# Performance work log

Measured on AMD Instinct MI355X. Metric: run time of the kernel, lower is better.

## Reference

```python
import jax, jax.numpy as jnp
import numpy as np

N_NODES = 50000
N_EDGES = 800000
IN_DIM = 256
OUT_DIM = 64
HEADS = 4
NEG_SLOPE = 0.2  # PyG GATConv default


def setup_inputs() -> dict:
    key = jax.random.key(0)
    k1, k2, k3, k4, k5, k6 = jax.random.split(key, 6)
    x = jax.random.normal(k1, (N_NODES, IN_DIM), dtype=jnp.float32)
    edge_index = jax.random.randint(k2, (2, N_EDGES), 0, N_NODES, dtype=jnp.int64)
    scale = 1.0 / np.sqrt(IN_DIM)
    W = jax.random.normal(k3, (IN_DIM, HEADS * OUT_DIM), dtype=jnp.float32) * scale
    att_src = jax.random.normal(k4, (HEADS, OUT_DIM), dtype=jnp.float32) * scale
    att_dst = jax.random.normal(k5, (HEADS, OUT_DIM), dtype=jnp.float32) * scale
    bias = jnp.zeros((HEADS * OUT_DIM,), dtype=jnp.float32)
    return {"x": x, "edge_index": edge_index, "W": W,
            "att_src": att_src, "att_dst": att_dst, "bias": bias}


def reference(x, edge_index, W, att_src, att_dst, bias):
    N = x.shape[0]
    H, C = att_src.shape
    # add self loops (PyG GATConv default add_self_loops=True)
    loop = jnp.arange(N, dtype=edge_index.dtype)
    src = jnp.concatenate([edge_index[0], loop])  # [E+N] source j
    dst = jnp.concatenate([edge_index[1], loop])  # [E+N] target i
    # linear projection, per-head features  [N, H, C]
    h = (x @ W).reshape(N, H, C)
    # attention logits: a_src . h_j + a_dst . h_i  -> [E, H]
    a_src = jnp.einsum('nhc,hc->nh', h, att_src)
    a_dst = jnp.einsum('nhc,hc->nh', h, att_dst)
    e = jax.nn.leaky_relu(a_src[src] + a_dst[dst], negative_slope=NEG_SLOPE)
    # edge softmax over incoming edges of each destination node
    m = jax.ops.segment_max(e, dst, num_segments=N)          # [N, H]
    p = jnp.exp(e - m[dst])                                  # [E, H]
    denom = jax.ops.segment_sum(p, dst, num_segments=N)      # [N, H]
    alpha = p / (denom[dst] + 1e-16)                         # [E, H]
    # weighted scatter-aggregate of gathered source features
    out = jax.ops.segment_sum(alpha[:, :, None] * h[src], dst, num_segments=N)
    out = out.reshape(N, H * C) + bias
    return jax.nn.relu(out)  # GATLayer active_func
```

## Files before the change

kernel.cpp:

```cpp
#include <hip/hip_runtime.h>

constexpr int N  = 50000;
constexpr int E  = 800000;
constexpr int K  = 256;
constexpr int F  = 256;
constexpr int H  = 4;
constexpr float SLOPE = 0.2f;

constexpr int CAPS = 6;

constexpr int NBK  = 98;
constexpr int BCAP = 16384;
constexpr int BKB  = 256;
constexpr int EPB  = E / BKB;

constexpr int WT_ROWS = 272;

constexpr size_t OFF_HB   = 0;
constexpr size_t OFF_WT   = OFF_HB   + (size_t)N * F * 2;
constexpr size_t OFF_ASRC = OFF_WT   + (size_t)WT_ROWS * K * 2;
constexpr size_t OFF_ADST = OFF_ASRC + (size_t)N * H * 4;
constexpr size_t OFF_DEG  = OFF_ADST + (size_t)N * H * 4;
constexpr size_t OFF_FLAG = OFF_DEG  + (size_t)N * 4;
constexpr size_t OFF_CSR  = OFF_FLAG + 64;
constexpr size_t OFF_BUF  = OFF_CSR  + (size_t)N * 64 * 4;
constexpr size_t OFF_GCUR = OFF_BUF  + (size_t)NBK * BCAP * 4;

constexpr int GEMM_TILES  = (N + 127) / 128;
constexpr int GEMM_BLOCKS = GEMM_TILES * 2;

typedef short short8 __attribute__((ext_vector_type(8)));
typedef float floatx4 __attribute__((ext_vector_type(4)));

__device__ __forceinline__ float leaky(float x) {
    return fmaxf(x, SLOPE * x);
}
__device__ __forceinline__ float blo(unsigned u) { return __uint_as_float(u << 16); }
__device__ __forceinline__ float bhi(unsigned u) { return __uint_as_float(u & 0xffff0000u); }
__device__ __forceinline__ unsigned short f2b(float f) {
    unsigned u = __float_as_uint(f);
    return (unsigned short)((u + 0x7fffu + ((u >> 16) & 1u)) >> 16);
}
__device__ __forceinline__ unsigned pk2(float a, float b) {
    return (unsigned)f2b(a) | ((unsigned)f2b(b) << 16);
}

__device__ __forceinline__ int edge_at(const void* ei, int is64, size_t i) {
    if (is64) return (int)((const long long*)ei)[i];
    return ((const int*)ei)[i];
}

__global__ __launch_bounds__(256)
void prep(const float* __restrict__ Wm, const float* __restrict__ att_src,
          const float* __restrict__ att_dst, const unsigned* __restrict__ ei_words,
          unsigned short* __restrict__ Wt, int* __restrict__ flag,
          int* __restrict__ gcur) {
    __shared__ float tile[64][65];
    __shared__ float as_l[64], ad_l[64];
    const int bid = blockIdx.x;
    const int t = threadIdx.x;
    if (bid < 16) {
        const int k0 = (bid & 3) * 64;
        const int n0 = (bid >> 2) * 64;
        const int r = t >> 2;
        const int c4 = (t & 3) * 16;
        #pragma unroll
        for (int i = 0; i < 16; i += 4) {
            float4 v = *reinterpret_cast<const float4*>(
                Wm + (size_t)(k0 + r) * F + n0 + c4 + i);
            tile[r][c4 + i + 0] = v.x;
            tile[r][c4 + i + 1] = v.y;
            tile[r][c4 + i + 2] = v.z;
            tile[r][c4 + i + 3] = v.w;
        }
        __syncthreads();
        unsigned pk[8];
        #pragma unroll
        for (int j = 0; j < 8; ++j)
            pk[j] = pk2(tile[c4 + 2 * j + 0][r], tile[c4 + 2 * j + 1][r]);
        unsigned short* dst = Wt + (size_t)(n0 + r) * K + k0 + c4;
        *reinterpret_cast<uint4*>(dst)     = make_uint4(pk[0], pk[1], pk[2], pk[3]);
        *reinterpret_cast<uint4*>(dst + 8) = make_uint4(pk[4], pk[5], pk[6], pk[7]);
    } else if (bid < 20) {
        const int h = bid - 16;
        if (t < 64) {
            as_l[t] = att_src[h * 64 + t];
            ad_l[t] = att_dst[h * 64 + t];
        }
        __syncthreads();
        const int k = t;
        const float* wr = Wm + (size_t)k * F + h * 64;
        float s = 0.f, d = 0.f;
        #pragma unroll
        for (int c = 0; c < 64; c += 4) {
            float4 w = *reinterpret_cast<const float4*>(wr + c);
            s += w.x * as_l[c] + w.y * as_l[c + 1]
               + w.z * as_l[c + 2] + w.w * as_l[c + 3];
            d += w.x * ad_l[c] + w.y * ad_l[c + 1]
               + w.z * ad_l[c + 2] + w.w * ad_l[c + 3];
        }
        Wt[(size_t)(256 + h) * K + k] = f2b(s);
        Wt[(size_t)(260 + h) * K + k] = f2b(d);
        if (h == 0) {
            #pragma unroll
            for (int r = 0; r < 8; ++r) Wt[(size_t)(264 + r) * K + k] = 0;
        }
    } else {
        if (t < 64) {
            unsigned v = ei_words[2 * t + 1];
            unsigned long long b = __ballot(v != 0u);
            if (t == 0) *flag = (b == 0ull) ? 1 : 0;
        }
        for (int j = t; j < NBK * 16; j += 256) gcur[j] = 0;
    }
}

constexpr int LDA = 72;
constexpr int LDW = 72;

__global__ __launch_bounds__(512, 4)
void gemm_hist(const float* __restrict__ X, const unsigned short* __restrict__ Wt,
               unsigned short* __restrict__ Hb, float* __restrict__ asrc,
               float* __restrict__ adst, const void* __restrict__ ei,
               const int* __restrict__ flag, unsigned* __restrict__ buf,
               int* __restrict__ gcur) {
    __shared__ unsigned short Al[128 * LDA];
    __shared__ unsigned short Wl[144 * LDW];
    const int tid = threadIdx.x;

    if (blockIdx.x < BKB) {
        int* cnt = (int*)(void*)Al;
        int* gsh = cnt + 128;
        int* scn = gsh + 128;
        unsigned* staged = (unsigned*)(void*)Wl;
        const int is64 = *flag;
        const int e0 = blockIdx.x * EPB;
        if (tid < 128) cnt[tid] = 0;
        __syncthreads();
        for (int it = 0; it < (EPB + 511) / 512; ++it) {
            int idx = it * 512 + tid;
            if (idx < EPB) {
                int d = edge_at(ei, is64, (size_t)E + e0 + idx);
                atomicAdd(&cnt[d >> 9], 1);
            }
        }
        __syncthreads();
        if (tid < 128) scn[tid] = cnt[tid];
        __syncthreads();
        for (int off = 1; off < 128; off <<= 1) {
            int v = 0;
            if (tid < 128 && tid >= off) v = scn[tid - off];
            __syncthreads();
            if (tid < 128) scn[tid] += v;
            __syncthreads();
        }
        if (tid < 128) {
            int c = cnt[tid];
            int lbase = scn[tid] - c;
            int gb = 0;
            if (c > 0 && tid < NBK) gb = atomicAdd(&gcur[tid * 16], c);
            gsh[tid] = gb - lbase;
            cnt[tid] = lbase;
        }
        __syncthreads();
        for (int it = 0; it < (EPB + 511) / 512; ++it) {
            int idx = it * 512 + tid;
            if (idx < EPB) {
                int d = edge_at(ei, is64, (size_t)E + e0 + idx);
                int s = edge_at(ei, is64, (size_t)(e0 + idx));
                int bk = d >> 9;
                int slot = atomicAdd(&cnt[bk], 1);
                staged[slot] = ((unsigned)bk << 25)
                             | ((unsigned)(d & 511) << 16) | (unsigned)s;
            }
        }
        __syncthreads();
        for (int j = tid; j < EPB; j += 512) {
            unsigned v = staged[j];
            int bk = (int)(v >> 25);
            buf[(size_t)bk * BCAP + gsh[bk] + j] = v;
        }
        return;
    }

    const int bid = blockIdx.x - BKB;
    const int tileR = bid >> 1;
    const int halfC = bid & 1;
    const int m0 = tileR * 128;
    const int c0 = halfC * 128;

    const int wv = tid >> 6, lane = tid & 63;
    const int quad = lane >> 4, l15 = lane & 15;
    const int rH = wv >> 2;
    const int cQ = wv & 3;
    const bool fusedw = (halfC == 1) && (cQ == 3);

    floatx4 acc[4][2];
    #pragma unroll
    for (int i = 0; i < 4; ++i)
        #pragma unroll
        for (int j = 0; j < 2; ++j) acc[i][j] = (floatx4)0.f;
    floatx4 accf[4];
    #pragma unroll
    for (int i = 0; i < 4; ++i) accf[i] = (floatx4)0.f;

    const int ar = tid >> 2;
    const int akc = (tid & 3) * 16;
    const bool arow_ok = (m0 + ar) < N;
    const int wr = tid >> 2;
    const int wkc = (tid & 3) * 16;

    for (int k0 = 0; k0 < K; k0 += 64) {
        {
            const float* src = X + (size_t)(m0 + ar) * K + k0 + akc;
            unsigned short* dst = &Al[ar * LDA + akc];
            #pragma unroll
            for (int i = 0; i < 16; i += 4) {
                float4 v = arow_ok ? *reinterpret_cast<const float4*>(src + i)
                                   : make_float4(0.f, 0.f, 0.f, 0.f);
                *reinterpret_cast<uint2*>(dst + i) =
                    make_uint2(pk2(v.x, v.y), pk2(v.z, v.w));
            }
        }
        {
            const unsigned short* src = Wt + (size_t)(c0 + wr) * K + k0 + wkc;
            unsigned short* dst = &Wl[wr * LDW + wkc];
            *reinterpret_cast<int4*>(dst)     = *reinterpret_cast<const int4*>(src);
            *reinterpret_cast<int4*>(dst + 8) = *reinterpret_cast<const int4*>(src + 8);
        }
        if (halfC == 1 && tid < 64) {
            const int fr = tid >> 2;
            const int fk = (tid & 3) * 16;
            const unsigned short* src = Wt + (size_t)(256 + fr) * K + k0 + fk;
            unsigned short* dst = &Wl[(128 + fr) * LDW + fk];
            *reinterpret_cast<int4*>(dst)     = *reinterpret_cast<const int4*>(src);
            *reinterpret_cast<int4*>(dst + 8) = *reinterpret_cast<const int4*>(src + 8);
        }
        __syncthreads();
        #pragma unroll
        for (int kk = 0; kk < 64; kk += 32) {
            short8 a[4];
            #pragma unroll
            for (int i = 0; i < 4; ++i)
                a[i] = *reinterpret_cast<const short8*>(
                    &Al[(rH * 64 + i * 16 + l15) * LDA + kk + quad * 8]);
            #pragma unroll
            for (int j = 0; j < 2; ++j) {
                short8 b = *reinterpret_cast<const short8*>(
                    &Wl[(cQ * 32 + j * 16 + l15) * LDW + kk + quad * 8]);
                #pragma unroll
                for (int i = 0; i < 4; ++i)
                    acc[i][j] = __builtin_amdgcn_mfma_f32_16x16x32_bf16(
                        a[i], b, acc[i][j], 0, 0, 0);
            }
            if (fusedw) {
                short8 bf = *reinterpret_cast<const short8*>(
                    &Wl[(128 + l15) * LDW + kk + quad * 8]);
                #pragma unroll
                for (int i = 0; i < 4; ++i)
                    accf[i] = __builtin_amdgcn_mfma_f32_16x16x32_bf16(
                        a[i], bf, accf[i], 0, 0, 0);
            }
        }
        __syncthreads();
    }
    #pragma unroll
    for (int i = 0; i < 4; ++i) {
        const int row = m0 + rH * 64 + i * 16 + quad * 4;
        #pragma unroll
        for (int j = 0; j < 2; ++j) {
            const int colb = c0 + cQ * 32 + j * 16;
            #pragma unroll
            for (int r = 0; r < 4; ++r) {
                float v = acc[i][j][r];
                float vn = __shfl_xor(v, 1);
                unsigned p = pk2(v, vn);
                unsigned q = __shfl_xor(p, 2);
                if ((l15 & 3) == 0 && (row + r) < N) {
                    *reinterpret_cast<uint2*>(
                        &Hb[(size_t)(row + r) * F + colb + l15]) =
                        make_uint2(p, q);
                }
            }
        }
    }
    if (fusedw) {
        #pragma unroll
        for (int i = 0; i < 4; ++i) {
            const int rbase = m0 + rH * 64 + i * 16 + quad * 4;
            #pragma unroll
            for (int r = 0; r < 4; ++r) {
                int row = rbase + r;
                if (row < N) {
                    if (l15 < 4)      asrc[row * H + l15] = accf[i][r];
                    else if (l15 < 8) adst[row * H + (l15 - 4)] = accf[i][r];
                }
            }
        }
    }
}

__global__ __launch_bounds__(1024)
void rank_scatter(const unsigned* __restrict__ buf, const int* __restrict__ gcur,
                  int* __restrict__ csr, int* __restrict__ deg) {
    __shared__ int h[512];
    const int b = blockIdx.x;
    const int t = threadIdx.x;
    if (t < 512) h[t] = 0;
    __syncthreads();
    const int nb = gcur[b * 16];
    for (int j = t; j < nb; j += 1024) {
        unsigned v = buf[(size_t)b * BCAP + j];
        int dl = (int)((v >> 16) & 511u);
        int s  = (int)(v & 0xffffu);
        int r = atomicAdd(&h[dl], 1);
        csr[(((b << 9) + dl) << CAPS) + r] = s;
    }
    __syncthreads();
    if (t < 512) {
        int n0 = (b << 9) + t;
        if (n0 < N) deg[n0] = h[t];
    }
}

__global__ __launch_bounds__(256, 8)
void aggregate(const unsigned short* __restrict__ Hb, const float* __restrict__ asrc,
               const float* __restrict__ adst, const int* __restrict__ deg,
               const int* __restrict__ csr, const float* __restrict__ bias,
               float* __restrict__ out) {
    const int wv = threadIdx.x >> 6;
    const int lane = threadIdx.x & 63;
    const int half = lane >> 5;
    const int l32 = lane & 31;
    const int hd = l32 >> 3;
    const int node = blockIdx.x * 4 + wv;

    const char* hbase = (const char*)Hb;
    const char* abase = (const char*)asrc;
    const unsigned lsh = (unsigned)l32 << 4;
    const unsigned hsh = (unsigned)hd << 2;

    const float adsti = adst[node * H + hd];
    const int start = node << CAPS;
    const int end = start + deg[node];

    float denom = 0.f;
    float a0 = 0.f, a1 = 0.f, a2 = 0.f, a3 = 0.f;
    float a4 = 0.f, a5 = 0.f, a6 = 0.f, a7 = 0.f;
    int e = start;
    for (; e + 8 <= end; e += 8) {
        unsigned s[4]; float l[4]; uint4 u[4];
        #pragma unroll
        for (int j = 0; j < 4; ++j) s[j] = (unsigned)csr[e + 2 * j + half];
        #pragma unroll
        for (int j = 0; j < 4; ++j)
            l[j] = *(const float*)(abase + ((s[j] << 4) + hsh));
        #pragma unroll
        for (int j = 0; j < 4; ++j)
            u[j] = *(const uint4*)(hbase + ((s[j] << 9) + lsh));
        #pragma unroll
        for (int j = 0; j < 4; ++j) {
            float p = __expf(leaky(l[j] + adsti));
            denom += p;
            a0 += p * blo(u[j].x); a1 += p * bhi(u[j].x);
            a2 += p * blo(u[j].y); a3 += p * bhi(u[j].y);
            a4 += p * blo(u[j].z); a5 += p * bhi(u[j].z);
            a6 += p * blo(u[j].w); a7 += p * bhi(u[j].w);
        }
    }
    for (; e + 2 <= end; e += 2) {
        unsigned s0 = (unsigned)csr[e + half];
        float l0 = *(const float*)(abase + ((s0 << 4) + hsh));
        uint4 u0 = *(const uint4*)(hbase + ((s0 << 9) + lsh));
        float p = __expf(leaky(l0 + adsti));
        denom += p;
        a0 += p * blo(u0.x); a1 += p * bhi(u0.x);
        a2 += p * blo(u0.y); a3 += p * bhi(u0.y);
        a4 += p * blo(u0.z); a5 += p * bhi(u0.z);
        a6 += p * blo(u0.w); a7 += p * bhi(u0.w);
    }
    {
        const int rem = end - e;
        bool active;
        unsigned sf;
        if (half == 0) { active = (rem == 1); sf = active ? (unsigned)csr[e] : 0u; }
        else           { active = true;       sf = (unsigned)node; }
        if (active) {
            float l0 = *(const float*)(abase + ((sf << 4) + hsh));
            uint4 u0 = *(const uint4*)(hbase + ((sf << 9) + lsh));
            float p = __expf(leaky(l0 + adsti));
            denom += p;
            a0 += p * blo(u0.x); a1 += p * bhi(u0.x);
            a2 += p * blo(u0.y); a3 += p * bhi(u0.y);
            a4 += p * blo(u0.z); a5 += p * bhi(u0.z);
            a6 += p * blo(u0.w); a7 += p * bhi(u0.w);
        }
    }
    a0 += __shfl_xor(a0, 32); a1 += __shfl_xor(a1, 32);
    a2 += __shfl_xor(a2, 32); a3 += __shfl_xor(a3, 32);
    a4 += __shfl_xor(a4, 32); a5 += __shfl_xor(a5, 32);
    a6 += __shfl_xor(a6, 32); a7 += __shfl_xor(a7, 32);
    denom += __shfl_xor(denom, 32);
    if (half == 0) {
        const float inv = 1.f / (denom + 1e-16f);
        float4 b0 = *reinterpret_cast<const float4*>(bias + l32 * 8);
        float4 b1 = *reinterpret_cast<const float4*>(bias + l32 * 8 + 4);
        float4 o0, o1;
        o0.x = fmaxf(a0 * inv + b0.x, 0.f);
        o0.y = fmaxf(a1 * inv + b0.y, 0.f);
        o0.z = fmaxf(a2 * inv + b0.z, 0.f);
        o0.w = fmaxf(a3 * inv + b0.w, 0.f);
        o1.x = fmaxf(a4 * inv + b1.x, 0.f);
        o1.y = fmaxf(a5 * inv + b1.y, 0.f);
        o1.z = fmaxf(a6 * inv + b1.z, 0.f);
        o1.w = fmaxf(a7 * inv + b1.w, 0.f);
        float* orow = out + (size_t)node * F + l32 * 8;
        *reinterpret_cast<float4*>(orow)     = o0;
        *reinterpret_cast<float4*>(orow + 4) = o1;
    }
}

extern "C" void kernel_launch(void* const* d_in, const int* in_sizes, int n_in,
                              void* d_out, int out_size, void* d_ws, size_t ws_size,
                              hipStream_t stream) {
    const float* x       = (const float*)d_in[0];
    const void*  ei      = d_in[1];
    const float* Wm      = (const float*)d_in[2];
    const float* att_src = (const float*)d_in[3];
    const float* att_dst = (const float*)d_in[4];
    const float* bias    = (const float*)d_in[5];
    float* out = (float*)d_out;

    char* ws = (char*)d_ws;
    unsigned short* hb = (unsigned short*)(ws + OFF_HB);
    unsigned short* wt = (unsigned short*)(ws + OFF_WT);
    float* asrc = (float*)(ws + OFF_ASRC);
    float* adst = (float*)(ws + OFF_ADST);
    int* deg  = (int*)(ws + OFF_DEG);
    int* flag = (int*)(ws + OFF_FLAG);
    int* csr  = (int*)(ws + OFF_CSR);
    unsigned* buf = (unsigned*)(ws + OFF_BUF);
    int* gcur = (int*)(ws + OFF_GCUR);

    prep<<<21, 256, 0, stream>>>(Wm, att_src, att_dst, (const unsigned*)ei,
                                 wt, flag, gcur);
    gemm_hist<<<BKB + GEMM_BLOCKS, 512, 0, stream>>>(
        x, wt, hb, asrc, adst, ei, flag, buf, gcur);
    rank_scatter<<<NBK, 1024, 0, stream>>>(buf, gcur, csr, deg);
    aggregate<<<N / 4, 256, 0, stream>>>(hb, asrc, adst, deg, csr, bias, out);
}
```

Measured before the change: 214.9 us.

## Restage pipeline: move edge bucketing into prep, fuse rank-scatter with GEMM

Edge bucketing moves from the GEMM kernel into the prep kernel, which also converts X to bf16 in a separate pass. The rank/scatter CSR build now runs as extra blocks of the GEMM kernel, so one launch is removed and CSR construction overlaps with the matmul. The GEMM then loads pre-converted bf16 X instead of converting fp32 on the fly, and gcur is zeroed with a memset. The trade-off is an extra full read and write of X (bf16 copy) and an extra memset call, plus a staged buffer that now sits in the smaller 256-thread block's shared tile.

```diff
diff --git a/kernel.cpp b/kernel.cpp
--- a/kernel.cpp
+++ b/kernel.cpp
@@ -21,13 +21,16 @@
 constexpr size_t OFF_ASRC = OFF_WT   + (size_t)WT_ROWS * K * 2;
 constexpr size_t OFF_ADST = OFF_ASRC + (size_t)N * H * 4;
 constexpr size_t OFF_DEG  = OFF_ADST + (size_t)N * H * 4;
-constexpr size_t OFF_FLAG = OFF_DEG  + (size_t)N * 4;
-constexpr size_t OFF_CSR  = OFF_FLAG + 64;
+constexpr size_t OFF_CSR  = OFF_DEG  + (size_t)N * 4 + 64;
 constexpr size_t OFF_BUF  = OFF_CSR  + (size_t)N * 64 * 4;
 constexpr size_t OFF_GCUR = OFF_BUF  + (size_t)NBK * BCAP * 4;
+constexpr size_t OFF_XB   = OFF_GCUR + (size_t)NBK * 16 * 4;
 
 constexpr int GEMM_TILES  = (N + 127) / 128;
 constexpr int GEMM_BLOCKS = GEMM_TILES * 2;
+
+constexpr int CVT_BLOCKS  = 1600;
+constexpr int PREP_BLOCKS = BKB + 20 + CVT_BLOCKS;
 
 typedef short short8 __attribute__((ext_vector_type(8)));
 typedef float floatx4 __attribute__((ext_vector_type(4)));
@@ -51,17 +54,73 @@
 }
 
 __global__ __launch_bounds__(256)
-void prep(const float* __restrict__ Wm, const float* __restrict__ att_src,
-          const float* __restrict__ att_dst, const unsigned* __restrict__ ei_words,
-          unsigned short* __restrict__ Wt, int* __restrict__ flag,
-          int* __restrict__ gcur) {
+void prep_all(const float* __restrict__ Wm, const float* __restrict__ att_src,
+              const float* __restrict__ att_dst, const void* __restrict__ ei,
+              const float* __restrict__ X, unsigned short* __restrict__ Wt,
+              unsigned short* __restrict__ Xb, unsigned* __restrict__ buf,
+              int* __restrict__ gcur) {
     __shared__ float tile[64][65];
     __shared__ float as_l[64], ad_l[64];
     const int bid = blockIdx.x;
     const int t = threadIdx.x;
-    if (bid < 16) {
-        const int k0 = (bid & 3) * 64;
-        const int n0 = (bid >> 2) * 64;
+    if (bid < BKB) {
+        const unsigned* ew = (const unsigned*)ei;
+        unsigned hw = ew[2 * (t & 63) + 1];
+        const int is64 = (__ballot(hw != 0u) == 0ull) ? 1 : 0;
+        int* cnt = (int*)(void*)tile;
+        int* gsh = cnt + 128;
+        int* scn = gsh + 128;
+        unsigned* staged = (unsigned*)(scn + 128);
+        const int e0 = bid * EPB;
+        if (t < 128) cnt[t] = 0;
+        __syncthreads();
+        for (int it = 0; it < (EPB + 255) / 256; ++it) {
+            int idx = it * 256 + t;
+            if (idx < EPB) {
+                int d = edge_at(ei, is64, (size_t)E + e0 + idx);
+                atomicAdd(&cnt[d >> 9], 1);
+            }
+        }
+        __syncthreads();
+        if (t < 128) scn[t] = cnt[t];
+        __syncthreads();
+        for (int off = 1; off < 128; off <<= 1) {
+            int v = 0;
+            if (t < 128 && t >= off) v = scn[t - off];
+            __syncthreads();
+            if (t < 128) scn[t] += v;
+            __syncthreads();
+        }
+        if (t < 128) {
+            int c = cnt[t];
+            int lbase = scn[t] - c;
+            int gb = 0;
+            if (c > 0 && t < NBK) gb = atomicAdd(&gcur[t * 16], c);
+            gsh[t] = gb - lbase;
+            cnt[t] = lbase;
+        }
+        __syncthreads();
+        for (int it = 0; it < (EPB + 255) / 256; ++it) {
+            int idx = it * 256 + t;
+            if (idx < EPB) {
+                int d = edge_at(ei, is64, (size_t)E + e0 + idx);
+                int s = edge_at(ei, is64, (size_t)(e0 + idx));
+                int bk = d >> 9;
+                int slot = atomicAdd(&cnt[bk], 1);
+                staged[slot] = ((unsigned)bk << 25)
+                             | ((unsigned)(d & 511) << 16) | (unsigned)s;
+            }
+        }
+        __syncthreads();
+        for (int j = t; j < EPB; j += 256) {
+            unsigned v = staged[j];
+            int bk = (int)(v >> 25);
+            buf[(size_t)bk * BCAP + gsh[bk] + j] = v;
+        }
+    } else if (bid < BKB + 16) {
+        const int tb = bid - BKB;
+        const int k0 = (tb & 3) * 64;
+        const int n0 = (tb >> 2) * 64;
         const int r = t >> 2;
         const int c4 = (t & 3) * 16;
         #pragma unroll
@@ -81,8 +140,8 @@
         unsigned short* dst = Wt + (size_t)(n0 + r) * K + k0 + c4;
         *reinterpret_cast<uint4*>(dst)     = make_uint4(pk[0], pk[1], pk[2], pk[3]);
         *reinterpret_cast<uint4*>(dst + 8) = make_uint4(pk[4], pk[5], pk[6], pk[7]);
-    } else if (bid < 20) {
-        const int h = bid - 16;
+    } else if (bid < BKB + 20) {
+        const int h = bid - (BKB + 16);
         if (t < 64) {
             as_l[t] = att_src[h * 64 + t];
             ad_l[t] = att_dst[h * 64 + t];
@@ -106,12 +165,15 @@
             for (int r = 0; r < 8; ++r) Wt[(size_t)(264 + r) * K + k] = 0;
         }
     } else {
-        if (t < 64) {
-            unsigned v = ei_words[2 * t + 1];
-            unsigned long long b = __ballot(v != 0u);
-            if (t == 0) *flag = (b == 0ull) ? 1 : 0;
-        }
-        for (int j = t; j < NBK * 16; j += 256) gcur[j] = 0;
+        const int cb = bid - (BKB + 20);
+        const float4* X4 = reinterpret_cast<const float4*>(X);
+        uint4* XB4 = reinterpret_cast<uint4*>(Xb);
+        const int NK8 = N * K / 8;
+        for (int u = cb * 256 + t; u < NK8; u += CVT_BLOCKS * 256) {
+            float4 a = X4[2 * u], b = X4[2 * u + 1];
+            XB4[u] = make_uint4(pk2(a.x, a.y), pk2(a.z, a.w),
+                                pk2(b.x, b.y), pk2(b.z, b.w));
+        }
     }
 }
 
@@ -119,71 +181,36 @@
 constexpr int LDW = 72;
 
 __global__ __launch_bounds__(512, 4)
-void gemm_hist(const float* __restrict__ X, const unsigned short* __restrict__ Wt,
+void gemm_rank(const unsigned short* __restrict__ Xb,
+               const unsigned short* __restrict__ Wt,
                unsigned short* __restrict__ Hb, float* __restrict__ asrc,
-               float* __restrict__ adst, const void* __restrict__ ei,
-               const int* __restrict__ flag, unsigned* __restrict__ buf,
-               int* __restrict__ gcur) {
+               float* __restrict__ adst, const unsigned* __restrict__ buf,
+               const int* __restrict__ gcur, int* __restrict__ csr,
+               int* __restrict__ deg) {
     __shared__ unsigned short Al[128 * LDA];
     __shared__ unsigned short Wl[144 * LDW];
     const int tid = threadIdx.x;
 
-    if (blockIdx.x < BKB) {
-        int* cnt = (int*)(void*)Al;
-        int* gsh = cnt + 128;
-        int* scn = gsh + 128;
-        unsigned* staged = (unsigned*)(void*)Wl;
-        const int is64 = *flag;
-        const int e0 = blockIdx.x * EPB;
-        if (tid < 128) cnt[tid] = 0;
-        __syncthreads();
-        for (int it = 0; it < (EPB + 511) / 512; ++it) {
-            int idx = it * 512 + tid;
-            if (idx < EPB) {
-                int d = edge_at(ei, is64, (size_t)E + e0 + idx);
-                atomicAdd(&cnt[d >> 9], 1);
-            }
-        }
-        __syncthreads();
-        if (tid < 128) scn[tid] = cnt[tid];
-        __syncthreads();
-        for (int off = 1; off < 128; off <<= 1) {
-            int v = 0;
-            if (tid < 128 && tid >= off) v = scn[tid - off];
-            __syncthreads();
-            if (tid < 128) scn[tid] += v;
-            __syncthreads();
-        }
-        if (tid < 128) {
-            int c = cnt[tid];
-            int lbase = scn[tid] - c;
-            int gb = 0;
-            if (c > 0 && tid < NBK) gb = atomicAdd(&gcur[tid * 16], c);
-            gsh[tid] = gb - lbase;
-            cnt[tid] = lbase;
-        }
-        __syncthreads();
-        for (int it = 0; it < (EPB + 511) / 512; ++it) {
-            int idx = it * 512 + tid;
-            if (idx < EPB) {
-                int d = edge_at(ei, is64, (size_t)E + e0 + idx);
-                int s = edge_at(ei, is64, (size_t)(e0 + idx));
-                int bk = d >> 9;
-                int slot = atomicAdd(&cnt[bk], 1);
-                staged[slot] = ((unsigned)bk << 25)
-                             | ((unsigned)(d & 511) << 16) | (unsigned)s;
-            }
-        }
-        __syncthreads();
-        for (int j = tid; j < EPB; j += 512) {
-            unsigned v = staged[j];
-            int bk = (int)(v >> 25);
-            buf[(size_t)bk * BCAP + gsh[bk] + j] = v;
-        }
+    if (blockIdx.x < NBK) {
+        int* h = (int*)(void*)Al;
+        h[tid] = 0;
+        __syncthreads();
+        const int b = blockIdx.x;
+        const int nb = gcur[b * 16];
+        for (int j = tid; j < nb; j += 512) {
+            unsigned v = buf[(size_t)b * BCAP + j];
+            int dl = (int)((v >> 16) & 511u);
+            int s  = (int)(v & 0xffffu);
+            int r = atomicAdd(&h[dl], 1);
+            csr[(((b << 9) + dl) << CAPS) + r] = s;
+        }
+        __syncthreads();
+        int n0 = (b << 9) + tid;
+        if (n0 < N) deg[n0] = h[tid];
         return;
     }
 
-    const int bid = blockIdx.x - BKB;
+    const int bid = blockIdx.x - NBK;
     const int tileR = bid >> 1;
     const int halfC = bid & 1;
     const int m0 = tileR * 128;
@@ -212,14 +239,14 @@
 
     for (int k0 = 0; k0 < K; k0 += 64) {
         {
-            const float* src = X + (size_t)(m0 + ar) * K + k0 + akc;
+            const unsigned short* src = Xb + (size_t)(m0 + ar) * K + k0 + akc;
             unsigned short* dst = &Al[ar * LDA + akc];
-            #pragma unroll
-            for (int i = 0; i < 16; i += 4) {
-                float4 v = arow_ok ? *reinterpret_cast<const float4*>(src + i)
-                                   : make_float4(0.f, 0.f, 0.f, 0.f);
-                *reinterpret_cast<uint2*>(dst + i) =
-                    make_uint2(pk2(v.x, v.y), pk2(v.z, v.w));
+            if (arow_ok) {
+                *reinterpret_cast<int4*>(dst)     = *reinterpret_cast<const int4*>(src);
+                *reinterpret_cast<int4*>(dst + 8) = *reinterpret_cast<const int4*>(src + 8);
+            } else {
+                *reinterpret_cast<int4*>(dst)     = make_int4(0, 0, 0, 0);
+                *reinterpret_cast<int4*>(dst + 8) = make_int4(0, 0, 0, 0);
             }
         }
         {
@@ -297,29 +324,6 @@
                 }
             }
         }
-    }
-}
-
-__global__ __launch_bounds__(1024)
-void rank_scatter(const unsigned* __restrict__ buf, const int* __restrict__ gcur,
-                  int* __restrict__ csr, int* __restrict__ deg) {
-    __shared__ int h[512];
-    const int b = blockIdx.x;
-    const int t = threadIdx.x;
-    if (t < 512) h[t] = 0;
-    __syncthreads();
-    const int nb = gcur[b * 16];
-    for (int j = t; j < nb; j += 1024) {
-        unsigned v = buf[(size_t)b * BCAP + j];
-        int dl = (int)((v >> 16) & 511u);
-        int s  = (int)(v & 0xffffu);
-        int r = atomicAdd(&h[dl], 1);
-        csr[(((b << 9) + dl) << CAPS) + r] = s;
-    }
-    __syncthreads();
-    if (t < 512) {
-        int n0 = (b << 9) + t;
-        if (n0 < N) deg[n0] = h[t];
     }
 }
 
@@ -437,15 +441,15 @@
     float* asrc = (float*)(ws + OFF_ASRC);
     float* adst = (float*)(ws + OFF_ADST);
     int* deg  = (int*)(ws + OFF_DEG);
-    int* flag = (int*)(ws + OFF_FLAG);
     int* csr  = (int*)(ws + OFF_CSR);
     unsigned* buf = (unsigned*)(ws + OFF_BUF);
     int* gcur = (int*)(ws + OFF_GCUR);
-
-    prep<<<21, 256, 0, stream>>>(Wm, att_src, att_dst, (const unsigned*)ei,
-                                 wt, flag, gcur);
-    gemm_hist<<<BKB + GEMM_BLOCKS, 512, 0, stream>>>(
-        x, wt, hb, asrc, adst, ei, flag, buf, gcur);
-    rank_scatter<<<NBK, 1024, 0, stream>>>(buf, gcur, csr, deg);
+    unsigned short* xb = (unsigned short*)(ws + OFF_XB);
+
+    hipMemsetAsync(ws + OFF_GCUR, 0, (size_t)NBK * 16 * 4, stream);
+    prep_all<<<PREP_BLOCKS, 256, 0, stream>>>(Wm, att_src, att_dst, ei, x,
+                                              wt, xb, buf, gcur);
+    gemm_rank<<<NBK + GEMM_BLOCKS, 512, 0, stream>>>(xb, wt, hb, asrc, adst,
+                                                     buf, gcur, csr, deg);
     aggregate<<<N / 4, 256, 0, stream>>>(hb, asrc, adst, deg, csr, bias, out);
 }
```

Result: no change. 213.8 us (-0.5%).
